# Kernel tuning notes

Hardware: AMD Instinct MI355X
Metric: run time of the kernel (lower is better)

Reference implementation:

```python
import jax, jax.numpy as jnp
import numpy as np
from jax import lax

B, T, D = 256, 512, 256          # batch, time, input_dim (neurons)
HE, HC, HG = 256, 256, 256       # encoder/controller/generator hidden
L, F = 64, 64                    # latent_dim, factor_dim


def gru_cell(x, h, Wih, Whh, bih, bhh):
    # PyTorch GRU gate order: r, z, n
    gi = x @ Wih.T + bih
    gh = h @ Whh.T + bhh
    ir, iz, inn = jnp.split(gi, 3, axis=-1)
    hr, hz, hn = jnp.split(gh, 3, axis=-1)
    r = jax.nn.sigmoid(ir + hr)
    z = jax.nn.sigmoid(iz + hz)
    n = jnp.tanh(inn + r * hn)
    return (1.0 - z) * n + z * h


def setup_inputs() -> dict:
    key = jax.random.key(0)
    ks = iter(jax.random.split(key, 40))
    def p(shape, scale=0.05):
        return (jax.random.normal(next(ks), shape, dtype=jnp.float32) * scale)
    inp = {
        "x": jax.random.normal(next(ks), (B, T, D), dtype=jnp.float32),
        "eps_u": jax.random.normal(next(ks), (T, B, L), dtype=jnp.float32),
        # bidirectional encoder GRU (forward / backward directions)
        "Wih_ef": p((3 * HE, D)), "Whh_ef": p((3 * HE, HE)), "bih_ef": p((3 * HE,)), "bhh_ef": p((3 * HE,)),
        "Wih_eb": p((3 * HE, D)), "Whh_eb": p((3 * HE, HE)), "bih_eb": p((3 * HE,)), "bhh_eb": p((3 * HE,)),
        # initial-condition heads
        "W_mu0": p((L, 2 * HE)), "b_mu0": p((L,)), "W_lv0": p((L, 2 * HE)), "b_lv0": p((L,)),
        # controller GRU + heads
        "Wih_c": p((3 * HC, D + F)), "Whh_c": p((3 * HC, HC)), "bih_c": p((3 * HC,)), "bhh_c": p((3 * HC,)),
        "W_cmu": p((L, HC)), "b_cmu": p((L,)), "W_clv": p((L, HC)), "b_clv": p((L,)),
        # generator GRU
        "Wih_g": p((3 * HG, L)), "Whh_g": p((3 * HG, HG)), "bih_g": p((3 * HG,)), "bhh_g": p((3 * HG,)),
        # readouts
        "W_f": p((F, HG)), "b_f": p((F,)), "W_r": p((D, F)), "b_r": p((D,)),
    }
    return inp


def reference(x, eps_u, Wih_ef, Whh_ef, bih_ef, bhh_ef, Wih_eb, Whh_eb, bih_eb, bhh_eb,
              W_mu0, b_mu0, W_lv0, b_lv0, Wih_c, Whh_c, bih_c, bhh_c,
              W_cmu, b_cmu, W_clv, b_clv, Wih_g, Whh_g, bih_g, bhh_g,
              W_f, b_f, W_r, b_r):
    xt = jnp.transpose(x, (1, 0, 2))  # [T, B, D]
    h0 = jnp.zeros((x.shape[0], HE), dtype=x.dtype)

    def enc_f(h, x_t):
        return gru_cell(x_t, h, Wih_ef, Whh_ef, bih_ef, bhh_ef), None

    def enc_b(h, x_t):
        return gru_cell(x_t, h, Wih_eb, Whh_eb, bih_eb, bhh_eb), None

    h_fwd, _ = lax.scan(enc_f, h0, xt)
    h_bwd, _ = lax.scan(enc_b, h0, xt, reverse=True)
    h_enc = jnp.concatenate([h_fwd, h_bwd], axis=-1)  # [B, 2*HE]

    mu0 = h_enc @ W_mu0.T + b_mu0
    lv0 = h_enc @ W_lv0.T + b_lv0
    kl_ics = (0.5 * jnp.sum(jnp.exp(lv0) + mu0 ** 2 - 1.0 - lv0, axis=1)).mean()
    # note: z0 is sampled in the original but never used (generator starts from zeros)

    c0 = jnp.zeros((x.shape[0], HC), dtype=x.dtype)
    g0 = jnp.zeros((x.shape[0], HG), dtype=x.dtype)
    f0 = jnp.zeros((x.shape[0], F), dtype=x.dtype)

    def step(carry, inputs):
        c_h, g_h, prev_f = carry
        x_t, eps_t = inputs
        c_in = jnp.concatenate([x_t, prev_f], axis=-1)  # [B, D+F]
        c_h = gru_cell(c_in, c_h, Wih_c, Whh_c, bih_c, bhh_c)
        mu_u = c_h @ W_cmu.T + b_cmu
        lv_u = c_h @ W_clv.T + b_clv
        u_t = mu_u + eps_t * jnp.exp(0.5 * lv_u)
        kl_t = (0.5 * jnp.sum(jnp.exp(lv_u) + mu_u ** 2 - 1.0 - lv_u, axis=1)).mean()
        g_h = gru_cell(u_t, g_h, Wih_g, Whh_g, bih_g, bhh_g)
        factors = g_h @ W_f.T + b_f
        rates_t = jnp.exp(factors @ W_r.T + b_r)
        return (c_h, g_h, factors), (rates_t, factors, kl_t)

    _, (rates, factors_all, kl_ts) = lax.scan(step, (c0, g0, f0), (xt, eps_u))
    rates = jnp.transpose(rates, (1, 0, 2))           # [B, T, D]
    factors_all = jnp.transpose(factors_all, (1, 0, 2))  # [B, T, F]
    kl_ctrl = kl_ts.mean()  # sum of per-step means / T
    return (rates, kl_ics, kl_ctrl, factors_all)
```

## Files before the change

### kernel.cpp

```cpp
#include <hip/hip_runtime.h>

typedef unsigned char u8;
typedef unsigned short u16;
typedef unsigned int u32;
typedef unsigned long long u64;
typedef short short8 __attribute__((ext_vector_type(8)));
typedef __bf16 bf16x8 __attribute__((ext_vector_type(8)));
typedef float f32x4 __attribute__((ext_vector_type(4)));
typedef float f32x2 __attribute__((ext_vector_type(2)));
typedef long longx2 __attribute__((ext_vector_type(2)));

#define DEV static __device__ __forceinline__

struct Params {
  const float *x, *eps;
  const float *Wih_ef, *Whh_ef, *bih_ef, *bhh_ef;
  const float *Wih_eb, *Whh_eb, *bih_eb, *bhh_eb;
  const float *W_mu0, *b_mu0, *W_lv0, *b_lv0;
  const float *Wih_c, *Whh_c, *bih_c, *bhh_c;
  const float *W_cmu, *b_cmu, *W_clv, *b_clv;
  const float *Wih_g, *Whh_g, *bih_g, *bhh_g;
  const float *W_f, *b_f, *W_r, *b_r;
  u8  *Xf8;
  u16 *ebf;
  u16 *wihcbf;
  float *bfc;
  u8 *wihef8, *whhef8, *wiheb8, *whheb8;
  u8 *whhc8, *whhg8;
  u8 *wihcf8, *wihg8;
  u8 *wf8, *wcmu8, *wclv8;
  u16 *wrbf;
  float *cbn;
  float *gb;
  float *hdb;
  float *fb2;
  float *eb;
  float *henc;
  float *klacc;
  float *klics;
  u8 *Gxc;
  float *out;
};

constexpr size_t RATES_N = 33554432ull;
constexpr size_t FOUT    = RATES_N + 2ull;

DEV u16 f2bf(float x) {
  unsigned u = __builtin_bit_cast(unsigned, x);
  u = (u + 0x7FFFu + ((u >> 16) & 1u)) >> 16;
  return (u16)u;
}
DEV float bf2f(u32 s) { return __builtin_bit_cast(float, s << 16); }
DEV unsigned f2e4m3(float x) {
  unsigned u = __builtin_bit_cast(unsigned, x);
  unsigned s = (u >> 24) & 0x80u;
  float ax = __builtin_bit_cast(float, u & 0x7FFFFFFFu);
  if (ax > 448.f) return s | 0x7E;
  if (ax < 0.0009765625f) return s;
  if (ax < 0.015625f) {
    int m = (int)rintf(ax * 512.f);
    if (m >= 8) return s | 0x08;
    return s | (unsigned)m;
  }
  unsigned au = __builtin_bit_cast(unsigned, ax);
  int E = (int)(au >> 23) - 127;
  unsigned m = au & 0x7FFFFFu;
  unsigned r = (m + 0x7FFFFu + ((m >> 20) & 1u)) >> 20;
  if (r >= 8) { r = 0; ++E; if (E > 8) return s | 0x7E; }
  return s | ((unsigned)(E + 7) << 3) | r;
}
DEV float e4m3tof(unsigned b) {
  unsigned s = (b & 0x80u) << 24;
  unsigned e = (b >> 3) & 15u, m = b & 7u;
  float v;
  if (e) v = __builtin_bit_cast(float, ((e + 120u) << 23) | (m << 20));
  else   v = (float)m * 0.001953125f;
  return __builtin_bit_cast(float, __builtin_bit_cast(unsigned, v) | s);
}
template <bool HI>
DEV unsigned pk2fp8(float a, float b, unsigned old) {
#if __has_builtin(__builtin_amdgcn_cvt_pk_fp8_f32)
  return (unsigned)__builtin_amdgcn_cvt_pk_fp8_f32(a, b, (int)old, HI);
#else
  unsigned p = f2e4m3(a) | (f2e4m3(b) << 8);
  return HI ? ((old & 0xFFFFu) | (p << 16)) : ((old & 0xFFFF0000u) | p);
#endif
}
template <bool HI>
DEV f32x2 pkf32(unsigned w) {
#if __has_builtin(__builtin_amdgcn_cvt_pk_f32_fp8)
  return __builtin_amdgcn_cvt_pk_f32_fp8((int)w, HI);
#else
  unsigned h = HI ? (w >> 16) : w;
  f32x2 r; r[0] = e4m3tof(h & 255u); r[1] = e4m3tof((h >> 8) & 255u); return r;
#endif
}
DEV float sigm(float x) { return 1.f / (1.f + __expf(-x)); }
DEV float ftanh(float x) { float t = __expf(2.f * x); return 1.f - 2.f / (t + 1.f); }
DEV float gru_h(float pr, float pz, float pin, float phn, float hp) {
  float r = sigm(pr), z = sigm(pz);
  float n = ftanh(pin + r * phn);
  return (1.f - z) * n + z * hp;
}
DEV u64 pack8f8(const float* s) {
  u64 p = 0;
  #pragma unroll
  for (int e = 0; e < 8; ++e) p |= (u64)f2e4m3(s[e]) << (8 * e);
  return p;
}

DEV f32x4 MFMA(short8 a, short8 b, f32x4 c) {
  return __builtin_amdgcn_mfma_f32_16x16x32_bf16(
      __builtin_bit_cast(bf16x8, a), __builtin_bit_cast(bf16x8, b), c, 0, 0, 0);
}
DEV f32x4 mfma8(long a, long b, f32x4 c) {
  return __builtin_amdgcn_mfma_f32_16x16x32_fp8_fp8(a, b, c, 0, 0, 0);
}
DEV short8 ldfrag(const u16* p0, int stride) {
  const int l = threadIdx.x & 63;
  const u16* p = p0 + (size_t)(l & 15) * stride + ((l >> 4) << 3);
  return *reinterpret_cast<const short8*>(p);
}
DEV short8 ldfrag_f32(const float* p0, int stride) {
  const int l = threadIdx.x & 63;
  const float* p = p0 + (size_t)(l & 15) * stride + ((l >> 4) << 3);
  f32x4 a = *reinterpret_cast<const f32x4*>(p);
  f32x4 b = *reinterpret_cast<const f32x4*>(p + 4);
  short8 r;
  r[0]=(short)f2bf(a[0]); r[1]=(short)f2bf(a[1]); r[2]=(short)f2bf(a[2]); r[3]=(short)f2bf(a[3]);
  r[4]=(short)f2bf(b[0]); r[5]=(short)f2bf(b[1]); r[6]=(short)f2bf(b[2]); r[7]=(short)f2bf(b[3]);
  return r;
}
DEV longx2 ldws2(const u8* w, int tile, int p) {
  return *(const longx2*)(w + ((size_t)tile << 12) + (p << 10) + ((threadIdx.x & 63) << 4));
}
DEV longx2 ldws64x(const u8* w, int tile) {
  return *(const longx2*)(w + ((size_t)tile << 10) + ((threadIdx.x & 63) << 4));
}
DEV int fragoff(int row, int jb) { return jb * 128 + ((row ^ (jb & 15)) << 3); }
DEV long ldsF(const u8* m, int r0, int rs, int kk) {
  int l = threadIdx.x & 63;
  int jb = kk * 4 + (l >> 4);
  return *(const long*)(m + ((r0 >> 4) << (rs + 4)) + fragoff(l & 15, jb));
}
DEV void stF(u8* m, int row, int col, unsigned v) {
  *(unsigned*)(m + fragoff(row, col >> 3) + (col & 7)) = v;
}
DEV short8 ldsB16(const u8* m, int r0, int kk) {
  int l = threadIdx.x & 63;
  int row = r0 + (l & 15);
  int off = row * 512 + kk * 64 + ((l >> 4) << 4);
  off ^= (row & 7) << 4;
  return *(const short8*)(m + off);
}
DEV void stage16(u8* dst, const u8* src, int nbytes) {
  for (int i = threadIdx.x * 16; i < nbytes; i += blockDim.x * 16) {
    int row = i >> 9;
    int off = i ^ ((row & 7) << 4);
    *(f32x4*)(dst + off) = *(const f32x4*)(src + i);
  }
}

__global__ __launch_bounds__(256) void k_init(Params P) {
  const size_t g  = (size_t)blockIdx.x * 256 + threadIdx.x;
  const size_t gs = (size_t)gridDim.x * 256;
  for (size_t i = g; i < 4194304ull; i += gs) {
    size_t flat = i << 3;
    int b = (int)(flat >> 17);
    int rem = (int)(flat & 131071);
    int t = rem >> 8, d = rem & 255;
    *(u64*)(P.Xf8 + (((size_t)t * 256 + b) << 8) + d) = pack8f8(P.x + flat);
  }
  for (size_t o = g; o < 1048576ull; o += gs) {
    int l = (int)(o & 63), k2 = (int)((o >> 6) & 1);
    int bt = (int)((o >> 7) & 15), t = (int)(o >> 11);
    int row = bt * 16 + (l & 15), col = k2 * 32 + ((l >> 4) << 3);
    const float* s = P.eps + ((size_t)t * 256 + row) * 64 + col;
    f32x4 v0 = *(const f32x4*)s, v1 = *(const f32x4*)(s + 4);
    short8 ob;
    ob[0]=(short)f2bf(v0[0]); ob[1]=(short)f2bf(v0[1]); ob[2]=(short)f2bf(v0[2]); ob[3]=(short)f2bf(v0[3]);
    ob[4]=(short)f2bf(v1[0]); ob[5]=(short)f2bf(v1[1]); ob[6]=(short)f2bf(v1[2]); ob[7]=(short)f2bf(v1[3]);
    *(short8*)((u8*)P.ebf + o * 16) = ob;
  }
  const int gi = (int)g, gsi = (int)gs;
  for (int i = gi; i < 24576; i += gsi) {
    int l = i & 63, kk = (i >> 6) & 7, tile = i >> 9;
    int row = tile * 16 + (l & 15), col = kk * 32 + ((l >> 4) << 3);
    size_t so = (size_t)row * 256 + col;
    size_t db = ((size_t)tile << 12) + ((kk >> 1) << 10) + (l << 4) + ((kk & 1) << 3);
    *(u64*)(P.whhc8  + db) = pack8f8(P.Whh_c  + so);
    *(u64*)(P.whhg8  + db) = pack8f8(P.Whh_g  + so);
    *(u64*)(P.wihef8 + db) = pack8f8(P.Wih_ef + so);
    *(u64*)(P.whhef8 + db) = pack8f8(P.Whh_ef + so);
    *(u64*)(P.wiheb8 + db) = pack8f8(P.Wih_eb + so);
    *(u64*)(P.whheb8 + db) = pack8f8(P.Whh_eb + so);
  }
  for (int i = gi; i < 2048; i += gsi) {
    int l = i & 63, kk = (i >> 6) & 7, tile = i >> 9;
    int row = tile * 16 + (l & 15), col = kk * 32 + ((l >> 4) << 3);
    size_t so = (size_t)row * 256 + col;
    size_t db = ((size_t)tile << 12) + ((kk >> 1) << 10) + (l << 4) + ((kk & 1) << 3);
    *(u64*)(P.wf8   + db) = pack8f8(P.W_f   + so);
    *(u64*)(P.wcmu8 + db) = pack8f8(P.W_cmu + so);
    *(u64*)(P.wclv8 + db) = pack8f8(P.W_clv + so);
  }
  for (int i = gi; i < 6144; i += gsi) {
    int l = i & 63, k2 = (i >> 6) & 1, tile = i >> 7;
    int row = tile * 16 + (l & 15), col = k2 * 32 + ((l >> 4) << 3);
    size_t db = ((size_t)tile << 10) + (l << 4) + (k2 << 3);
    *(u64*)(P.wihcf8 + db) = pack8f8(P.Wih_c + (size_t)row * 320 + 256 + col);
    *(u64*)(P.wihg8  + db) = pack8f8(P.Wih_g + (size_t)row * 64 + col);
  }
  for (int i = gi; i < 196608; i += gsi) {
    int r = i >> 8, c = i & 255;
    P.wihcbf[i] = f2bf(P.Wih_c[r * 320 + c]);
  }
  for (int i = gi; i < 16384; i += gsi) P.wrbf[i] = f2bf(P.W_r[i]);
  for (int i = gi; i < 768; i += gsi)
    P.bfc[i] = P.bih_c[i] + (i < 512 ? P.bhh_c[i] : 0.f);
  for (int i = gi; i < 256; i += gsi) {
    P.cbn[i] = P.bhh_c[512 + i];
    P.gb[i]        = P.bih_g[i] + P.bhh_g[i];
    P.gb[256 + i]  = P.bih_g[256 + i] + P.bhh_g[256 + i];
    P.gb[512 + i]  = P.bih_g[512 + i];
    P.gb[768 + i]  = P.bhh_g[512 + i];
    P.eb[i]        = P.bih_ef[i] + P.bhh_ef[i];
    P.eb[256 + i]  = P.bih_ef[256 + i] + P.bhh_ef[256 + i];
    P.eb[512 + i]  = P.bih_ef[512 + i];
    P.eb[768 + i]  = P.bhh_ef[512 + i];
    P.eb[1024 + i] = P.bih_eb[i] + P.bhh_eb[i];
    P.eb[1280 + i] = P.bih_eb[256 + i] + P.bhh_eb[256 + i];
    P.eb[1536 + i] = P.bih_eb[512 + i];
    P.eb[1792 + i] = P.bhh_eb[512 + i];
  }
  for (int i = gi; i < 128; i += gsi) P.hdb[i] = (i < 64) ? P.b_cmu[i] : P.b_clv[i - 64];
  for (int i = gi; i < 64; i += gsi)  P.fb2[i] = P.b_f[i];
}

__global__ __launch_bounds__(512, 2) void k_gx(Params P) {
  extern __shared__ char smem[];
  u8* sA = (u8*)smem;
  u8* sB = sA + 65536;
  const int nc = blockIdx.x % 6;
  const int tb = blockIdx.x / 6;
  const int t = tb >> 1, bh = tb & 1;
  stage16(sA, (const u8*)(P.wihcbf + (size_t)nc * 128 * 256), 65536);
  for (int i = threadIdx.x * 8; i < 32768; i += 512 * 8) {
    int r = i >> 8, c = i & 255;
    const float* s = P.x + ((size_t)(bh * 128 + r) * 512 + t) * 256 + c;
    f32x4 v0 = *(const f32x4*)s, v1 = *(const f32x4*)(s + 4);
    short8 o;
    o[0]=(short)f2bf(v0[0]); o[1]=(short)f2bf(v0[1]); o[2]=(short)f2bf(v0[2]); o[3]=(short)f2bf(v0[3]);
    o[4]=(short)f2bf(v1[0]); o[5]=(short)f2bf(v1[1]); o[6]=(short)f2bf(v1[2]); o[7]=(short)f2bf(v1[3]);
    int off = (r * 512 + c * 2) ^ ((r & 7) << 4);
    *(short8*)(sB + off) = o;
  }
  __syncthreads();
  const int lane = threadIdx.x & 63, wid = threadIdx.x >> 6;
  const int rq = (lane >> 4) << 2;
  const int nglob = nc * 128 + wid * 16;
  short8 Af[8];
  #pragma unroll
  for (int kk = 0; kk < 8; ++kk) Af[kk] = ldsB16(sA, wid * 16, kk);
  float bq[4];
  #pragma unroll
  for (int q = 0; q < 4; ++q) bq[q] = P.bfc[nglob + rq + q];
  #pragma unroll 1
  for (int bt = 0; bt < 8; ++bt) {
    f32x4 acc = {0.f, 0.f, 0.f, 0.f};
    #pragma unroll
    for (int kk = 0; kk < 8; ++kk)
      acc = MFMA(Af[kk], ldsB16(sB, bt * 16, kk), acc);
    float v0 = acc[0] + bq[0], v1 = acc[1] + bq[1], v2 = acc[2] + bq[2], v3 = acc[3] + bq[3];
    unsigned pw = pk2fp8<false>(v0, v1, 0u); pw = pk2fp8<true>(v2, v3, pw);
    *(u32*)(P.Gxc + (((size_t)(t * 16 + bh * 8 + bt) * 48 + (nglob >> 4)) << 8) + (lane << 2)) = pw;
  }
}

DEV void cg_role(const Params& P, int blk, char* smem) {
  u8* hc8  = (u8*)smem;
  u8* hg8  = hc8 + 8192;
  u8* f8b  = hg8 + 8192;
  float* sml  = (float*)(f8b + 2048);
  float* sred = sml + 16 * 132;

  const int lane = threadIdx.x & 63, wid = threadIdx.x >> 6;
  const int cl = lane & 15, rq = (lane >> 4) << 2;
  const int b0 = blk << 4, j0 = wid << 5, jt = wid << 1;
  const int sel = wid >> 2, l0 = (wid & 3) << 4;

  for (int i = threadIdx.x * 4; i < 18432; i += 512 * 4) *(int*)(hc8 + i) = 0;

  f32x4 bnv[2], brv[2], bzv[2], biv[2], bhv2[2];
  #pragma unroll
  for (int c2 = 0; c2 < 2; ++c2) {
    int j = j0 + c2 * 16 + rq;
    bnv[c2]  = *(const f32x4*)(P.cbn + j);
    brv[c2]  = *(const f32x4*)(P.gb + j);
    bzv[c2]  = *(const f32x4*)(P.gb + 256 + j);
    biv[c2]  = *(const f32x4*)(P.gb + 512 + j);
    bhv2[c2] = *(const f32x4*)(P.gb + 768 + j);
  }
  f32x4 hbv = *(const f32x4*)(P.hdb + sel * 64 + l0 + rq);
  f32x4 fbv = {0, 0, 0, 0};
  if (wid < 4) fbv = *(const f32x4*)(P.fb2 + wid * 16 + rq);

  f32x4 hcM[2] = {{0,0,0,0},{0,0,0,0}};
  f32x4 hgM[2] = {{0,0,0,0},{0,0,0,0}};
  float klv = 0.f;
  __syncthreads();

  #pragma unroll 1
  for (int t = 0; t < 512; ++t) {
    const int cur = t & 1, prv = cur ^ 1;
    u8 *hcP = hc8 + prv * 4096, *hcC = hc8 + cur * 4096;
    u8 *hgP = hg8 + prv * 4096, *hgC = hg8 + cur * 4096;
    int zz = 0; asm volatile("" : "+v"(zz));
    const u8* wcS = P.whhc8 + zz;
    const u8* wgS = P.whhg8 + zz;
    const u8* cfS = P.wihcf8 + zz;
    const u8* guS = P.wihg8 + zz;
    const u8* hdS = (sel ? P.wclv8 : P.wcmu8) + zz;
    const u8* wfS = P.wf8 + zz;
    u32 gx[6];
    { const u8* gp = P.Gxc + (((size_t)(t * 16 + blk) * 48) << 8) + (lane << 2);
      #pragma unroll
      for (int c2 = 0; c2 < 2; ++c2)
        #pragma unroll
        for (int g3 = 0; g3 < 3; ++g3)
          gx[c2 * 3 + g3] = *(const u32*)(gp + ((g3 * 16 + jt + c2) << 8));
    }
    short8 ee0 = *(const short8*)((const u8*)P.ebf + (((size_t)(t * 16 + blk) * 2 + 0) << 10) + lane * 16);
    short8 ee1 = *(const short8*)((const u8*)P.ebf + (((size_t)(t * 16 + blk) * 2 + 1) << 10) + lane * 16);
    long hf[8];
    #pragma unroll
    for (int kk = 0; kk < 8; ++kk) hf[kk] = ldsF(hcP, 0, 8, kk);
    long ff0 = ldsF(f8b + prv * 1024, 0, 6, 0);
    long ff1 = ldsF(f8b + prv * 1024, 0, 6, 1);
    #pragma unroll
    for (int c2 = 0; c2 < 2; ++c2) {
      longx2 w0[4], w1[4], w2[4];
      #pragma unroll
      for (int p = 0; p < 4; ++p) {
        w0[p] = ldws2(wcS,      jt + c2, p);
        w1[p] = ldws2(wcS, 16 + jt + c2, p);
        w2[p] = ldws2(wcS, 32 + jt + c2, p);
      }
      longx2 cf0 = ldws64x(cfS,      jt + c2);
      longx2 cf1 = ldws64x(cfS, 16 + jt + c2);
      longx2 cf2 = ldws64x(cfS, 32 + jt + c2);
      f32x4 ar = {0,0,0,0}, az = {0,0,0,0}, ai = {0,0,0,0}, ah = {0,0,0,0};
      #pragma unroll
      for (int p = 0; p < 4; ++p) {
        ar = mfma8(w0[p].x, hf[2*p], ar);  ar = mfma8(w0[p].y, hf[2*p+1], ar);
        az = mfma8(w1[p].x, hf[2*p], az);  az = mfma8(w1[p].y, hf[2*p+1], az);
        ah = mfma8(w2[p].x, hf[2*p], ah);  ah = mfma8(w2[p].y, hf[2*p+1], ah);
      }
      ar = mfma8(cf0.x, ff0, ar); ar = mfma8(cf0.y, ff1, ar);
      az = mfma8(cf1.x, ff0, az); az = mfma8(cf1.y, ff1, az);
      ai = mfma8(cf2.x, ff0, ai); ai = mfma8(cf2.y, ff1, ai);
      f32x2 rlo = pkf32<false>(gx[c2*3+0]), rhi = pkf32<true>(gx[c2*3+0]);
      f32x2 zlo = pkf32<false>(gx[c2*3+1]), zhi = pkf32<true>(gx[c2*3+1]);
      f32x2 nlo = pkf32<false>(gx[c2*3+2]), nhi = pkf32<true>(gx[c2*3+2]);
      f32x4 bn = bnv[c2];
      float h0 = gru_h(ar[0]+rlo[0], az[0]+zlo[0], ai[0]+nlo[0], ah[0]+bn[0], hcM[c2][0]);
      float h1 = gru_h(ar[1]+rlo[1], az[1]+zlo[1], ai[1]+nlo[1], ah[1]+bn[1], hcM[c2][1]);
      float h2 = gru_h(ar[2]+rhi[0], az[2]+zhi[0], ai[2]+nhi[0], ah[2]+bn[2], hcM[c2][2]);
      float h3 = gru_h(ar[3]+rhi[1], az[3]+zhi[1], ai[3]+nhi[1], ah[3]+bn[3], hcM[c2][3]);
      hcM[c2][0] = h0; hcM[c2][1] = h1; hcM[c2][2] = h2; hcM[c2][3] = h3;
      unsigned pw = pk2fp8<false>(h0, h1, 0u); pw = pk2fp8<true>(h2, h3, pw);
      stF(hcC, cl, j0 + c2 * 16 + rq, pw);
    }
    __syncthreads();
    { long hcv[8];
      #pragma unroll
      for (int kk = 0; kk < 8; ++kk) hcv[kk] = ldsF(hcC, 0, 8, kk);
      f32x4 am = {0,0,0,0};
      #pragma unroll
      for (int p = 0; p < 4; ++p) {
        longx2 wp = ldws2(hdS, wid & 3, p);
        am = mfma8(wp.x, hcv[2*p], am);
        am = mfma8(wp.y, hcv[2*p+1], am);
      }
      am += hbv;
      *(f32x4*)(sml + cl * 132 + sel * 64 + l0 + rq) = am;
    }
    __syncthreads();
    long U[2];
    { const float* ml = sml + cl * 132;
      const int kh = (lane >> 4) << 3;
      #pragma unroll
      for (int k2 = 0; k2 < 2; ++k2) {
        f32x4 mu0 = *(const f32x4*)(ml + k2 * 32 + kh);
        f32x4 mu1 = *(const f32x4*)(ml + k2 * 32 + kh + 4);
        f32x4 lv0 = *(const f32x4*)(ml + 64 + k2 * 32 + kh);
        f32x4 lv1 = *(const f32x4*)(ml + 64 + k2 * 32 + kh + 4);
        short8 ev = k2 ? ee1 : ee0;
        float uu[8];
        #pragma unroll
        for (int e = 0; e < 4; ++e) {
          float epv = bf2f((u32)(u16)ev[e]);
          uu[e] = mu0[e] + epv * __expf(0.5f * lv0[e]);
        }
        #pragma unroll
        for (int e = 0; e < 4; ++e) {
          float epv = bf2f((u32)(u16)ev[4 + e]);
          uu[4 + e] = mu1[e] + epv * __expf(0.5f * lv1[e]);
        }
        unsigned pa = pk2fp8<false>(uu[0], uu[1], 0u); pa = pk2fp8<true>(uu[2], uu[3], pa);
        unsigned pb = pk2fp8<false>(uu[4], uu[5], 0u); pb = pk2fp8<true>(uu[6], uu[7], pb);
        U[k2] = (long)(((u64)pb << 32) | (u64)pa);
      }
    }
    long hg[8];
    #pragma unroll
    for (int kk = 0; kk < 8; ++kk) hg[kk] = ldsF(hgP, 0, 8, kk);
    #pragma unroll
    for (int c2 = 0; c2 < 2; ++c2) {
      longx2 g0[4], g1[4], g2[4];
      #pragma unroll
      for (int p = 0; p < 4; ++p) {
        g0[p] = ldws2(wgS,      jt + c2, p);
        g1[p] = ldws2(wgS, 16 + jt + c2, p);
        g2[p] = ldws2(wgS, 32 + jt + c2, p);
      }
      longx2 u0 = ldws64x(guS,      jt + c2);
      longx2 u1 = ldws64x(guS, 16 + jt + c2);
      longx2 u2 = ldws64x(guS, 32 + jt + c2);
      f32x4 gr = {0,0,0,0}, gz = {0,0,0,0}, gi = {0,0,0,0}, gh = {0,0,0,0};
      #pragma unroll
      for (int p = 0; p < 4; ++p) {
        gr = mfma8(g0[p].x, hg[2*p], gr);  gr = mfma8(g0[p].y, hg[2*p+1], gr);
        gz = mfma8(g1[p].x, hg[2*p], gz);  gz = mfma8(g1[p].y, hg[2*p+1], gz);
        gh = mfma8(g2[p].x, hg[2*p], gh);  gh = mfma8(g2[p].y, hg[2*p+1], gh);
      }
      gr = mfma8(u0.x, U[0], gr); gr = mfma8(u0.y, U[1], gr);
      gz = mfma8(u1.x, U[0], gz); gz = mfma8(u1.y, U[1], gz);
      gi = mfma8(u2.x, U[0], gi); gi = mfma8(u2.y, U[1], gi);
      float h0 = gru_h(gr[0]+brv[c2][0], gz[0]+bzv[c2][0], gi[0]+biv[c2][0], gh[0]+bhv2[c2][0], hgM[c2][0]);
      float h1 = gru_h(gr[1]+brv[c2][1], gz[1]+bzv[c2][1], gi[1]+biv[c2][1], gh[1]+bhv2[c2][1], hgM[c2][1]);
      float h2 = gru_h(gr[2]+brv[c2][2], gz[2]+bzv[c2][2], gi[2]+biv[c2][2], gh[2]+bhv2[c2][2], hgM[c2][2]);
      float h3 = gru_h(gr[3]+brv[c2][3], gz[3]+bzv[c2][3], gi[3]+biv[c2][3], gh[3]+bhv2[c2][3], hgM[c2][3]);
      hgM[c2][0] = h0; hgM[c2][1] = h1; hgM[c2][2] = h2; hgM[c2][3] = h3;
      unsigned pw = pk2fp8<false>(h0, h1, 0u); pw = pk2fp8<true>(h2, h3, pw);
      stF(hgC, cl, j0 + c2 * 16 + rq, pw);
    }
    __syncthreads();
    if (wid < 4) {
      long hgv[8];
      #pragma unroll
      for (int kk = 0; kk < 8; ++kk) hgv[kk] = ldsF(hgC, 0, 8, kk);
      f32x4 af = {0,0,0,0};
      #pragma unroll
      for (int p = 0; p < 4; ++p) {
        longx2 wp = ldws2(wfS, wid, p);
        af = mfma8(wp.x, hgv[2*p], af);
        af = mfma8(wp.y, hgv[2*p+1], af);
      }
      af += fbv;
      float* fo = P.out + FOUT + (size_t)(b0 + cl) * 32768 + (size_t)t * 64 + wid * 16 + rq;
      f32x2 lo = {af[0], af[1]}, hi2 = {af[2], af[3]};
      *(f32x2*)fo = lo;
      *(f32x2*)(fo + 2) = hi2;
      unsigned pw = pk2fp8<false>(af[0], af[1], 0u); pw = pk2fp8<true>(af[2], af[3], pw);
      stF(f8b + cur * 1024, cl, wid * 16 + rq, pw);
    } else {
      #pragma unroll
      for (int e = 0; e < 4; ++e) {
        int p = ((wid - 4) * 64 + lane) * 4 + e;
        int row = p >> 6, l = p & 63;
        float mu = sml[row * 132 + l], lv = sml[row * 132 + 64 + l];
        klv += __expf(lv) + mu * mu - 1.f - lv;
      }
    }
    __syncthreads();
  }
  if (wid >= 4) {
    float v = klv;
    v += __shfl_down(v, 32); v += __shfl_down(v, 16); v += __shfl_down(v, 8);
    v += __shfl_down(v, 4);  v += __shfl_down(v, 2);  v += __shfl_down(v, 1);
    if (lane == 0) sred[wid] = v;
  }
  __syncthreads();
  if (threadIdx.x == 0) P.klacc[blk] = sred[4] + sred[5] + sred[6] + sred[7];
}

DEV void enc_role(const Params& P, int dir, int b0, char* smem) {
  u8* h8 = (u8*)smem;
  u8* sx = h8 + 8192;
  const int lane = threadIdx.x & 63, wid = threadIdx.x >> 6;
  const int cl = lane & 15, rq = (lane >> 4) << 2;
  const int j0 = wid << 5, jt = wid << 1;
  const u8* wihS0 = dir ? P.wiheb8 : P.wihef8;
  const u8* whhS0 = dir ? P.whheb8 : P.whhef8;
  const float* ebt = P.eb + dir * 1024;
  for (int i = threadIdx.x * 4; i < 8192; i += 512 * 4) *(int*)(h8 + i) = 0;
  f32x4 brv[2], bzv[2], biv[2], bhv2[2];
  #pragma unroll
  for (int c2 = 0; c2 < 2; ++c2) {
    int j = j0 + c2 * 16 + rq;
    brv[c2]  = *(const f32x4*)(ebt + j);
    bzv[c2]  = *(const f32x4*)(ebt + 256 + j);
    biv[c2]  = *(const f32x4*)(ebt + 512 + j);
    bhv2[c2] = *(const f32x4*)(ebt + 768 + j);
  }
  f32x4 heM[2] = {{0,0,0,0},{0,0,0,0}};
  const int ssrc = threadIdx.x * 8;
  const int sdst = fragoff(threadIdx.x >> 5, threadIdx.x & 31);
  const int t0 = dir ? 511 : 0;
  *(u64*)(sx + sdst) = *(const u64*)(P.Xf8 + (((size_t)t0 * 256 + b0) << 8) + ssrc);
  __syncthreads();

  #pragma unroll 1
  for (int i = 0; i < 512; ++i) {
    const int cur = i & 1, prv = cur ^ 1;
    const int t = dir ? (511 - i) : i;
    u8 *hP = h8 + prv * 4096, *hC = h8 + cur * 4096;
    const u8* sxc = sx + cur * 4096;
    int zz = 0; asm volatile("" : "+v"(zz));
    const u8* wihS = wihS0 + zz;
    const u8* whhS = whhS0 + zz;
    u64 xpre = 0;
    if (i < 511) {
      int tn = dir ? (t - 1) : (t + 1);
      xpre = *(const u64*)(P.Xf8 + (((size_t)tn * 256 + b0) << 8) + ssrc);
    }
    long hp[8], xv[8];
    #pragma unroll
    for (int kk = 0; kk < 8; ++kk) { hp[kk] = ldsF(hP, 0, 8, kk); xv[kk] = ldsF(sxc, 0, 8, kk); }
    #pragma unroll
    for (int c2 = 0; c2 < 2; ++c2) {
      longx2 H0[4], H1[4], H2[4], I0[4], I1[4], I2[4];
      #pragma unroll
      for (int p = 0; p < 4; ++p) {
        H0[p] = ldws2(whhS,      jt + c2, p);
        H1[p] = ldws2(whhS, 16 + jt + c2, p);
        H2[p] = ldws2(whhS, 32 + jt + c2, p);
        I0[p] = ldws2(wihS,      jt + c2, p);
        I1[p] = ldws2(wihS, 16 + jt + c2, p);
        I2[p] = ldws2(wihS, 32 + jt + c2, p);
      }
      f32x4 er = {0,0,0,0}, ez = {0,0,0,0}, ei = {0,0,0,0}, eh = {0,0,0,0};
      #pragma unroll
      for (int p = 0; p < 4; ++p) {
        er = mfma8(H0[p].x, hp[2*p], er);  er = mfma8(H0[p].y, hp[2*p+1], er);
        ez = mfma8(H1[p].x, hp[2*p], ez);  ez = mfma8(H1[p].y, hp[2*p+1], ez);
        eh = mfma8(H2[p].x, hp[2*p], eh);  eh = mfma8(H2[p].y, hp[2*p+1], eh);
        er = mfma8(I0[p].x, xv[2*p], er);  er = mfma8(I0[p].y, xv[2*p+1], er);
        ez = mfma8(I1[p].x, xv[2*p], ez);  ez = mfma8(I1[p].y, xv[2*p+1], ez);
        ei = mfma8(I2[p].x, xv[2*p], ei);  ei = mfma8(I2[p].y, xv[2*p+1], ei);
      }
      float h0 = gru_h(er[0]+brv[c2][0], ez[0]+bzv[c2][0], ei[0]+biv[c2][0], eh[0]+bhv2[c2][0], heM[c2][0]);
      float h1 = gru_h(er[1]+brv[c2][1], ez[1]+bzv[c2][1], ei[1]+biv[c2][1], eh[1]+bhv2[c2][1], heM[c2][1]);
      float h2 = gru_h(er[2]+brv[c2][2], ez[2]+bzv[c2][2], ei[2]+biv[c2][2], eh[2]+bhv2[c2][2], heM[c2][2]);
      float h3 = gru_h(er[3]+brv[c2][3], ez[3]+bzv[c2][3], ei[3]+biv[c2][3], eh[3]+bhv2[c2][3], heM[c2][3]);
      heM[c2][0] = h0; heM[c2][1] = h1; heM[c2][2] = h2; heM[c2][3] = h3;
      unsigned pw = pk2fp8<false>(h0, h1, 0u); pw = pk2fp8<true>(h2, h3, pw);
      stF(hC, cl, j0 + c2 * 16 + rq, pw);
    }
    if (i < 511) *(u64*)(sx + prv * 4096 + sdst) = xpre;
    __syncthreads();
  }
  #pragma unroll
  for (int c2 = 0; c2 < 2; ++c2)
    *(f32x4*)(P.henc + (size_t)(dir * 256 + b0 + cl) * 256 + j0 + c2 * 16 + rq) = heM[c2];
}

__global__ __launch_bounds__(512, 2) void k_main(Params P) {
  extern __shared__ char smem[];
  const int blk = blockIdx.x;
  if (blk < 16) cg_role(P, blk, smem);
  else {
    const int e = blk - 16;
    enc_role(P, e >> 4, (e & 15) << 4, smem);
  }
}

__global__ __launch_bounds__(256) void k_post(Params P) {
  const int blk = blockIdx.x;
  if (blk < 32) {
    __shared__ float red[4];
    float ka = 0.f;
    #pragma unroll 1
    for (int pp = 0; pp < 2; ++pp) {
      int p = blk * 512 + threadIdx.x * 2 + pp;
      int b = p >> 6, l = p & 63;
      float mu = P.b_mu0[l], lv = P.b_lv0[l];
      const float* wm = P.W_mu0 + (size_t)l * 512;
      const float* wl = P.W_lv0 + (size_t)l * 512;
      const float* h0 = P.henc + (size_t)b * 256;
      const float* h1 = P.henc + (size_t)(256 + b) * 256;
      #pragma unroll 4
      for (int k = 0; k < 256; ++k) {
        float hf = h0[k], hb = h1[k];
        mu += hf * wm[k] + hb * wm[256 + k];
        lv += hf * wl[k] + hb * wl[256 + k];
      }
      ka += __expf(lv) + mu * mu - 1.f - lv;
    }
    const int lane = threadIdx.x & 63, wid = threadIdx.x >> 6;
    ka += __shfl_down(ka, 32); ka += __shfl_down(ka, 16); ka += __shfl_down(ka, 8);
    ka += __shfl_down(ka, 4);  ka += __shfl_down(ka, 2);  ka += __shfl_down(ka, 1);
    if (lane == 0) red[wid] = ka;
    __syncthreads();
    if (threadIdx.x == 0) P.klics[blk] = red[0] + red[1] + red[2] + red[3];
  } else {
    const int lane = threadIdx.x & 63, wid = threadIdx.x >> 6;
    const int cl = lane & 15, rq = (lane >> 4) << 2;
    const int gw = (blk - 32) * 4 + wid;
    const size_t r0 = (size_t)gw << 4;
    const float* Fs = P.out + FOUT;
    short8 F0 = ldfrag_f32(Fs + r0 * 64, 64);
    short8 F1 = ldfrag_f32(Fs + r0 * 64 + 32, 64);
    #pragma unroll 1
    for (int ct = 0; ct < 16; ++ct) {
      const int d0 = ct << 4;
      const u16* W = P.wrbf + (size_t)d0 * 64;
      f32x4 a = {0,0,0,0};
      a = MFMA(ldfrag(W, 64), F0, a);
      a = MFMA(ldfrag(W + 32, 64), F1, a);
      f32x4 rb = *(const f32x4*)(P.b_r + d0 + rq);
      f32x4 o;
      o[0] = __expf(a[0] + rb[0]); o[1] = __expf(a[1] + rb[1]);
      o[2] = __expf(a[2] + rb[2]); o[3] = __expf(a[3] + rb[3]);
      *(f32x4*)(P.out + (r0 + cl) * 256 + d0 + rq) = o;
    }
  }
}

__global__ void k_final(Params P) {
  if (threadIdx.x == 0) {
    float s = 0.f, s2 = 0.f;
    for (int i = 0; i < 16; ++i) s += P.klacc[i];
    for (int i = 0; i < 32; ++i) s2 += P.klics[i];
    P.out[RATES_N]     = s2 * (0.5f / 256.f);
    P.out[RATES_N + 1] = s  * (0.5f / (256.f * 512.f));
  }
}

extern "C" void kernel_launch(void* const* d_in, const int* in_sizes, int n_in,
                              void* d_out, int out_size, void* d_ws, size_t ws_size,
                              hipStream_t stream) {
  (void)in_sizes; (void)n_in; (void)out_size; (void)ws_size;
  Params P;
  const float* const* in = (const float* const*)d_in;
  P.x = in[0];      P.eps = in[1];
  P.Wih_ef = in[2]; P.Whh_ef = in[3]; P.bih_ef = in[4]; P.bhh_ef = in[5];
  P.Wih_eb = in[6]; P.Whh_eb = in[7]; P.bih_eb = in[8]; P.bhh_eb = in[9];
  P.W_mu0 = in[10]; P.b_mu0 = in[11]; P.W_lv0 = in[12]; P.b_lv0 = in[13];
  P.Wih_c = in[14]; P.Whh_c = in[15]; P.bih_c = in[16]; P.bhh_c = in[17];
  P.W_cmu = in[18]; P.b_cmu = in[19]; P.W_clv = in[20]; P.b_clv = in[21];
  P.Wih_g = in[22]; P.Whh_g = in[23]; P.bih_g = in[24]; P.bhh_g = in[25];
  P.W_f = in[26];   P.b_f = in[27];   P.W_r = in[28];   P.b_r = in[29];

  char* w = (char*)d_ws;
  size_t off = 0;
  auto take = [&](size_t bytes) -> char* {
    char* r = w + off;
    off = (off + bytes + 255) & ~(size_t)255;
    return r;
  };
  P.Xf8    = (u8*)take(33554432ull);
  P.ebf    = (u16*)take(16777216ull * 2);
  P.wihcbf = (u16*)take(196608ull * 2);
  P.bfc    = (float*)take(768ull * 4);
  P.wihef8 = (u8*)take(196608ull);
  P.whhef8 = (u8*)take(196608ull);
  P.wiheb8 = (u8*)take(196608ull);
  P.whheb8 = (u8*)take(196608ull);
  P.whhc8  = (u8*)take(196608ull);
  P.whhg8  = (u8*)take(196608ull);
  P.wihcf8 = (u8*)take(49152ull);
  P.wihg8  = (u8*)take(49152ull);
  P.wf8    = (u8*)take(16384ull);
  P.wcmu8  = (u8*)take(16384ull);
  P.wclv8  = (u8*)take(16384ull);
  P.wrbf   = (u16*)take(16384ull * 2);
  P.cbn    = (float*)take(256ull * 4);
  P.gb     = (float*)take(1024ull * 4);
  P.hdb    = (float*)take(128ull * 4);
  P.fb2    = (float*)take(64ull * 4);
  P.eb     = (float*)take(2048ull * 4);
  P.henc   = (float*)take(131072ull * 4);
  P.klacc  = (float*)take(64ull * 4);
  P.klics  = (float*)take(64ull * 4);
  P.Gxc    = (u8*)d_out;
  P.out    = (float*)d_out;

  hipLaunchKernelGGL(k_init,  dim3(2048), dim3(256), 0, stream, P);
  hipLaunchKernelGGL(k_gx,    dim3(6144), dim3(512), 131072, stream, P);
  hipLaunchKernelGGL(k_main,  dim3(48),   dim3(512), 27008, stream, P);
  hipLaunchKernelGGL(k_post,  dim3(2080), dim3(256), 0, stream, P);
  hipLaunchKernelGGL(k_final, dim3(1),    dim3(64),  0, stream, P);
}
```

Baseline: 4.712 ms.

## Issue per-step weight loads as inline-asm batches with explicit vmcnt wait

Replaces the compiler-generated per-step weight fetches in the controller, generator, head and encoder GRU loops with inline-asm global_load_dwordx4 batches. Each batch is followed by one s_waitcnt vmcnt(0) plus a sched barrier, and the controller loads now sit ahead of the LDS reads. This drops the zero-register trick that forced reloads and aims to overlap all weight-load latency with the LDS fragment reads. It raises register pressure by holding about 24 longx2 weight registers at once, and changes the launch-bounds attribute to amdgpu_waves_per_eu(2,2).

```diff
diff --git a/kernel.cpp b/kernel.cpp
--- a/kernel.cpp
+++ b/kernel.cpp
@@ -131,11 +131,20 @@
   r[4]=(short)f2bf(b[0]); r[5]=(short)f2bf(b[1]); r[6]=(short)f2bf(b[2]); r[7]=(short)f2bf(b[3]);
   return r;
 }
-DEV longx2 ldws2(const u8* w, int tile, int p) {
-  return *(const longx2*)(w + ((size_t)tile << 12) + (p << 10) + ((threadIdx.x & 63) << 4));
-}
-DEV longx2 ldws64x(const u8* w, int tile) {
-  return *(const longx2*)(w + ((size_t)tile << 10) + ((threadIdx.x & 63) << 4));
+DEV longx2 aload(const u8* p) {
+  longx2 r;
+  asm volatile("global_load_dwordx4 %0, %1, off" : "=v"(r) : "v"(p));
+  return r;
+}
+DEV void vwait0() {
+  asm volatile("s_waitcnt vmcnt(0)" ::: "memory");
+  __builtin_amdgcn_sched_barrier(0);
+}
+DEV const u8* wsaddr(const u8* w, int tile, int p) {
+  return w + ((size_t)tile << 12) + (p << 10) + ((threadIdx.x & 63) << 4);
+}
+DEV const u8* ws64addr(const u8* w, int tile) {
+  return w + ((size_t)tile << 10) + ((threadIdx.x & 63) << 4);
 }
 DEV int fragoff(int row, int jb) { return jb * 128 + ((row ^ (jb & 15)) << 3); }
 DEV long ldsF(const u8* m, int r0, int rs, int kk) {
@@ -303,7 +312,7 @@
   }
   f32x4 hbv = *(const f32x4*)(P.hdb + sel * 64 + l0 + rq);
   f32x4 fbv = {0, 0, 0, 0};
-  if (wid < 4) fbv = *(const f32x4*)(P.fb2 + wid * 16 + rq);
+  if (wid < 4) fbv = *(const f32x4*)(P.fb2 + (wid << 4) + rq);
 
   f32x4 hcM[2] = {{0,0,0,0},{0,0,0,0}};
   f32x4 hgM[2] = {{0,0,0,0},{0,0,0,0}};
@@ -315,13 +324,6 @@
     const int cur = t & 1, prv = cur ^ 1;
     u8 *hcP = hc8 + prv * 4096, *hcC = hc8 + cur * 4096;
     u8 *hgP = hg8 + prv * 4096, *hgC = hg8 + cur * 4096;
-    int zz = 0; asm volatile("" : "+v"(zz));
-    const u8* wcS = P.whhc8 + zz;
-    const u8* wgS = P.whhg8 + zz;
-    const u8* cfS = P.wihcf8 + zz;
-    const u8* guS = P.wihg8 + zz;
-    const u8* hdS = (sel ? P.wclv8 : P.wcmu8) + zz;
-    const u8* wfS = P.wf8 + zz;
     u32 gx[6];
     { const u8* gp = P.Gxc + (((size_t)(t * 16 + blk) * 48) << 8) + (lane << 2);
       #pragma unroll
@@ -332,33 +334,34 @@
     }
     short8 ee0 = *(const short8*)((const u8*)P.ebf + (((size_t)(t * 16 + blk) * 2 + 0) << 10) + lane * 16);
     short8 ee1 = *(const short8*)((const u8*)P.ebf + (((size_t)(t * 16 + blk) * 2 + 1) << 10) + lane * 16);
+    longx2 wc[6][4], cfv[6];
+    #pragma unroll
+    for (int c2 = 0; c2 < 2; ++c2)
+      #pragma unroll
+      for (int g3 = 0; g3 < 3; ++g3) {
+        #pragma unroll
+        for (int p = 0; p < 4; ++p)
+          wc[c2 * 3 + g3][p] = aload(wsaddr(P.whhc8, g3 * 16 + jt + c2, p));
+        cfv[c2 * 3 + g3] = aload(ws64addr(P.wihcf8, g3 * 16 + jt + c2));
+      }
     long hf[8];
     #pragma unroll
     for (int kk = 0; kk < 8; ++kk) hf[kk] = ldsF(hcP, 0, 8, kk);
     long ff0 = ldsF(f8b + prv * 1024, 0, 6, 0);
     long ff1 = ldsF(f8b + prv * 1024, 0, 6, 1);
+    vwait0();
     #pragma unroll
     for (int c2 = 0; c2 < 2; ++c2) {
-      longx2 w0[4], w1[4], w2[4];
+      f32x4 ar = {0,0,0,0}, az = {0,0,0,0}, ai = {0,0,0,0}, ah = {0,0,0,0};
       #pragma unroll
       for (int p = 0; p < 4; ++p) {
-        w0[p] = ldws2(wcS,      jt + c2, p);
-        w1[p] = ldws2(wcS, 16 + jt + c2, p);
-        w2[p] = ldws2(wcS, 32 + jt + c2, p);
-      }
-      longx2 cf0 = ldws64x(cfS,      jt + c2);
-      longx2 cf1 = ldws64x(cfS, 16 + jt + c2);
-      longx2 cf2 = ldws64x(cfS, 32 + jt + c2);
-      f32x4 ar = {0,0,0,0}, az = {0,0,0,0}, ai = {0,0,0,0}, ah = {0,0,0,0};
-      #pragma unroll
-      for (int p = 0; p < 4; ++p) {
-        ar = mfma8(w0[p].x, hf[2*p], ar);  ar = mfma8(w0[p].y, hf[2*p+1], ar);
-        az = mfma8(w1[p].x, hf[2*p], az);  az = mfma8(w1[p].y, hf[2*p+1], az);
-        ah = mfma8(w2[p].x, hf[2*p], ah);  ah = mfma8(w2[p].y, hf[2*p+1], ah);
-      }
-      ar = mfma8(cf0.x, ff0, ar); ar = mfma8(cf0.y, ff1, ar);
-      az = mfma8(cf1.x, ff0, az); az = mfma8(cf1.y, ff1, az);
-      ai = mfma8(cf2.x, ff0, ai); ai = mfma8(cf2.y, ff1, ai);
+        ar = mfma8(wc[c2*3+0][p].x, hf[2*p], ar);  ar = mfma8(wc[c2*3+0][p].y, hf[2*p+1], ar);
+        az = mfma8(wc[c2*3+1][p].x, hf[2*p], az);  az = mfma8(wc[c2*3+1][p].y, hf[2*p+1], az);
+        ah = mfma8(wc[c2*3+2][p].x, hf[2*p], ah);  ah = mfma8(wc[c2*3+2][p].y, hf[2*p+1], ah);
+      }
+      ar = mfma8(cfv[c2*3+0].x, ff0, ar); ar = mfma8(cfv[c2*3+0].y, ff1, ar);
+      az = mfma8(cfv[c2*3+1].x, ff0, az); az = mfma8(cfv[c2*3+1].y, ff1, az);
+      ai = mfma8(cfv[c2*3+2].x, ff0, ai); ai = mfma8(cfv[c2*3+2].y, ff1, ai);
       f32x2 rlo = pkf32<false>(gx[c2*3+0]), rhi = pkf32<true>(gx[c2*3+0]);
       f32x2 zlo = pkf32<false>(gx[c2*3+1]), zhi = pkf32<true>(gx[c2*3+1]);
       f32x2 nlo = pkf32<false>(gx[c2*3+2]), nhi = pkf32<true>(gx[c2*3+2]);
@@ -372,20 +375,35 @@
       stF(hcC, cl, j0 + c2 * 16 + rq, pw);
     }
     __syncthreads();
-    { long hcv[8];
+    {
+      longx2 hd[4];
+      const u8* hdS = sel ? P.wclv8 : P.wcmu8;
+      #pragma unroll
+      for (int p = 0; p < 4; ++p) hd[p] = aload(wsaddr(hdS, wid & 3, p));
+      long hcv[8];
       #pragma unroll
       for (int kk = 0; kk < 8; ++kk) hcv[kk] = ldsF(hcC, 0, 8, kk);
+      vwait0();
       f32x4 am = {0,0,0,0};
       #pragma unroll
       for (int p = 0; p < 4; ++p) {
-        longx2 wp = ldws2(hdS, wid & 3, p);
-        am = mfma8(wp.x, hcv[2*p], am);
-        am = mfma8(wp.y, hcv[2*p+1], am);
+        am = mfma8(hd[p].x, hcv[2*p], am);
+        am = mfma8(hd[p].y, hcv[2*p+1], am);
       }
       am += hbv;
       *(f32x4*)(sml + cl * 132 + sel * 64 + l0 + rq) = am;
     }
     __syncthreads();
+    longx2 wg[6][4], gu[6];
+    #pragma unroll
+    for (int c2 = 0; c2 < 2; ++c2)
+      #pragma unroll
+      for (int g3 = 0; g3 < 3; ++g3) {
+        #pragma unroll
+        for (int p = 0; p < 4; ++p)
+          wg[c2 * 3 + g3][p] = aload(wsaddr(P.whhg8, g3 * 16 + jt + c2, p));
+        gu[c2 * 3 + g3] = aload(ws64addr(P.wihg8, g3 * 16 + jt + c2));
+      }
     long U[2];
     { const float* ml = sml + cl * 132;
       const int kh = (lane >> 4) << 3;
@@ -415,28 +433,19 @@
     long hg[8];
     #pragma unroll
     for (int kk = 0; kk < 8; ++kk) hg[kk] = ldsF(hgP, 0, 8, kk);
+    vwait0();
     #pragma unroll
     for (int c2 = 0; c2 < 2; ++c2) {
-      longx2 g0[4], g1[4], g2[4];
+      f32x4 gr = {0,0,0,0}, gz = {0,0,0,0}, gi = {0,0,0,0}, gh = {0,0,0,0};
       #pragma unroll
       for (int p = 0; p < 4; ++p) {
-        g0[p] = ldws2(wgS,      jt + c2, p);
-        g1[p] = ldws2(wgS, 16 + jt + c2, p);
-        g2[p] = ldws2(wgS, 32 + jt + c2, p);
-      }
-      longx2 u0 = ldws64x(guS,      jt + c2);
-      longx2 u1 = ldws64x(guS, 16 + jt + c2);
-      longx2 u2 = ldws64x(guS, 32 + jt + c2);
-      f32x4 gr = {0,0,0,0}, gz = {0,0,0,0}, gi = {0,0,0,0}, gh = {0,0,0,0};
-      #pragma unroll
-      for (int p = 0; p < 4; ++p) {
-        gr = mfma8(g0[p].x, hg[2*p], gr);  gr = mfma8(g0[p].y, hg[2*p+1], gr);
-        gz = mfma8(g1[p].x, hg[2*p], gz);  gz = mfma8(g1[p].y, hg[2*p+1], gz);
-        gh = mfma8(g2[p].x, hg[2*p], gh);  gh = mfma8(g2[p].y, hg[2*p+1], gh);
-      }
-      gr = mfma8(u0.x, U[0], gr); gr = mfma8(u0.y, U[1], gr);
-      gz = mfma8(u1.x, U[0], gz); gz = mfma8(u1.y, U[1], gz);
-      gi = mfma8(u2.x, U[0], gi); gi = mfma8(u2.y, U[1], gi);
+        gr = mfma8(wg[c2*3+0][p].x, hg[2*p], gr);  gr = mfma8(wg[c2*3+0][p].y, hg[2*p+1], gr);
+        gz = mfma8(wg[c2*3+1][p].x, hg[2*p], gz);  gz = mfma8(wg[c2*3+1][p].y, hg[2*p+1], gz);
+        gh = mfma8(wg[c2*3+2][p].x, hg[2*p], gh);  gh = mfma8(wg[c2*3+2][p].y, hg[2*p+1], gh);
+      }
+      gr = mfma8(gu[c2*3+0].x, U[0], gr); gr = mfma8(gu[c2*3+0].y, U[1], gr);
+      gz = mfma8(gu[c2*3+1].x, U[0], gz); gz = mfma8(gu[c2*3+1].y, U[1], gz);
+      gi = mfma8(gu[c2*3+2].x, U[0], gi); gi = mfma8(gu[c2*3+2].y, U[1], gi);
       float h0 = gru_h(gr[0]+brv[c2][0], gz[0]+bzv[c2][0], gi[0]+biv[c2][0], gh[0]+bhv2[c2][0], hgM[c2][0]);
       float h1 = gru_h(gr[1]+brv[c2][1], gz[1]+bzv[c2][1], gi[1]+biv[c2][1], gh[1]+bhv2[c2][1], hgM[c2][1]);
       float h2 = gru_h(gr[2]+brv[c2][2], gz[2]+bzv[c2][2], gi[2]+biv[c2][2], gh[2]+bhv2[c2][2], hgM[c2][2]);
@@ -447,15 +456,18 @@
     }
     __syncthreads();
     if (wid < 4) {
+      longx2 wfv[4];
+      #pragma unroll
+      for (int p = 0; p < 4; ++p) wfv[p] = aload(wsaddr(P.wf8, wid, p));
       long hgv[8];
       #pragma unroll
       for (int kk = 0; kk < 8; ++kk) hgv[kk] = ldsF(hgC, 0, 8, kk);
+      vwait0();
       f32x4 af = {0,0,0,0};
       #pragma unroll
       for (int p = 0; p < 4; ++p) {
-        longx2 wp = ldws2(wfS, wid, p);
-        af = mfma8(wp.x, hgv[2*p], af);
-        af = mfma8(wp.y, hgv[2*p+1], af);
+        af = mfma8(wfv[p].x, hgv[2*p], af);
+        af = mfma8(wfv[p].y, hgv[2*p+1], af);
       }
       af += fbv;
       float* fo = P.out + FOUT + (size_t)(b0 + cl) * 32768 + (size_t)t * 64 + wid * 16 + rq;
@@ -517,9 +529,6 @@
     const int t = dir ? (511 - i) : i;
     u8 *hP = h8 + prv * 4096, *hC = h8 + cur * 4096;
     const u8* sxc = sx + cur * 4096;
-    int zz = 0; asm volatile("" : "+v"(zz));
-    const u8* wihS = wihS0 + zz;
-    const u8* whhS = whhS0 + zz;
     u64 xpre = 0;
     if (i < 511) {
       int tn = dir ? (t - 1) : (t + 1);
@@ -530,25 +539,24 @@
     for (int kk = 0; kk < 8; ++kk) { hp[kk] = ldsF(hP, 0, 8, kk); xv[kk] = ldsF(sxc, 0, 8, kk); }
     #pragma unroll
     for (int c2 = 0; c2 < 2; ++c2) {
-      longx2 H0[4], H1[4], H2[4], I0[4], I1[4], I2[4];
+      longx2 Hw[3][4], Iw[3][4];
+      #pragma unroll
+      for (int g3 = 0; g3 < 3; ++g3)
+        #pragma unroll
+        for (int p = 0; p < 4; ++p) {
+          Hw[g3][p] = aload(wsaddr(whhS0, g3 * 16 + jt + c2, p));
+          Iw[g3][p] = aload(wsaddr(wihS0, g3 * 16 + jt + c2, p));
+        }
+      vwait0();
+      f32x4 er = {0,0,0,0}, ez = {0,0,0,0}, ei = {0,0,0,0}, eh = {0,0,0,0};
       #pragma unroll
       for (int p = 0; p < 4; ++p) {
-        H0[p] = ldws2(whhS,      jt + c2, p);
-        H1[p] = ldws2(whhS, 16 + jt + c2, p);
-        H2[p] = ldws2(whhS, 32 + jt + c2, p);
-        I0[p] = ldws2(wihS,      jt + c2, p);
-        I1[p] = ldws2(wihS, 16 + jt + c2, p);
-        I2[p] = ldws2(wihS, 32 + jt + c2, p);
-      }
-      f32x4 er = {0,0,0,0}, ez = {0,0,0,0}, ei = {0,0,0,0}, eh = {0,0,0,0};
-      #pragma unroll
-      for (int p = 0; p < 4; ++p) {
-        er = mfma8(H0[p].x, hp[2*p], er);  er = mfma8(H0[p].y, hp[2*p+1], er);
-        ez = mfma8(H1[p].x, hp[2*p], ez);  ez = mfma8(H1[p].y, hp[2*p+1], ez);
-        eh = mfma8(H2[p].x, hp[2*p], eh);  eh = mfma8(H2[p].y, hp[2*p+1], eh);
-        er = mfma8(I0[p].x, xv[2*p], er);  er = mfma8(I0[p].y, xv[2*p+1], er);
-        ez = mfma8(I1[p].x, xv[2*p], ez);  ez = mfma8(I1[p].y, xv[2*p+1], ez);
-        ei = mfma8(I2[p].x, xv[2*p], ei);  ei = mfma8(I2[p].y, xv[2*p+1], ei);
+        er = mfma8(Hw[0][p].x, hp[2*p], er);  er = mfma8(Hw[0][p].y, hp[2*p+1], er);
+        ez = mfma8(Hw[1][p].x, hp[2*p], ez);  ez = mfma8(Hw[1][p].y, hp[2*p+1], ez);
+        eh = mfma8(Hw[2][p].x, hp[2*p], eh);  eh = mfma8(Hw[2][p].y, hp[2*p+1], eh);
+        er = mfma8(Iw[0][p].x, xv[2*p], er);  er = mfma8(Iw[0][p].y, xv[2*p+1], er);
+        ez = mfma8(Iw[1][p].x, xv[2*p], ez);  ez = mfma8(Iw[1][p].y, xv[2*p+1], ez);
+        ei = mfma8(Iw[2][p].x, xv[2*p], ei);  ei = mfma8(Iw[2][p].y, xv[2*p+1], ei);
       }
       float h0 = gru_h(er[0]+brv[c2][0], ez[0]+bzv[c2][0], ei[0]+biv[c2][0], eh[0]+bhv2[c2][0], heM[c2][0]);
       float h1 = gru_h(er[1]+brv[c2][1], ez[1]+bzv[c2][1], ei[1]+biv[c2][1], eh[1]+bhv2[c2][1], heM[c2][1]);
@@ -566,7 +574,9 @@
     *(f32x4*)(P.henc + (size_t)(dir * 256 + b0 + cl) * 256 + j0 + c2 * 16 + rq) = heM[c2];
 }
 
-__global__ __launch_bounds__(512, 2) void k_main(Params P) {
+__global__ __launch_bounds__(512)
+__attribute__((amdgpu_waves_per_eu(2, 2)))
+void k_main(Params P) {
   extern __shared__ char smem[];
   const int blk = blockIdx.x;
   if (blk < 16) cg_role(P, blk, smem);
```

Measured after the change: 9.658 ms. 105% more time.
